# Kernel optimization log

Measured on AMD Instinct MI355X. Metric: run time of the kernel, lower is better.

Reference implementation:

```python
import jax, jax.numpy as jnp
import numpy as np

H = 2048
Q_RANK = 256
SCALE = float(np.sqrt(Q_RANK))


def setup_inputs() -> dict:
    key = jax.random.key(0)
    k_x, k_s, k_a, k_o, k_b = jax.random.split(key, 5)
    B, L = 4, 4096
    x = jax.random.normal(k_x, (B, L, H), dtype=jnp.float32)
    # nn.Linear(H, q_rank, bias=False): weight [q_rank, H]; y = x @ W.T -> store transposed [H, q_rank]
    Ws = jax.random.normal(k_s, (H, Q_RANK), dtype=jnp.float32) / np.sqrt(H)
    Wa = jax.random.normal(k_a, (H, Q_RANK), dtype=jnp.float32) / np.sqrt(H)
    Wo = jax.random.normal(k_o, (H, H), dtype=jnp.float32) / np.sqrt(H)
    bo = jax.random.normal(k_b, (H,), dtype=jnp.float32) * 0.01
    return {"x": x, "Ws": Ws, "Wa": Wa, "Wo": Wo, "bo": bo}


def reference(x, Ws, Wa, Wo, bo):
    # x: [B, L, H]
    B, L, _ = x.shape
    state = jnp.einsum('blh,hr->blr', x, Ws)   # [B, L, r]
    action = jnp.einsum('blh,hr->blr', x, Wa)  # [B, L, r]
    q_values = jnp.einsum('bir,bjr->bij', state, action) / SCALE  # [B, L, L]
    # causal mask: position i attends to j <= i
    causal = jnp.tril(jnp.ones((L, L), dtype=bool))
    q_values = jnp.where(causal, q_values, -jnp.inf)
    weights = jax.nn.softmax(q_values, axis=-1)  # [B, L, L]
    out = jnp.einsum('bij,bjh->bih', weights, x)  # weights @ x (x acts as V)
    return jnp.einsum('bih,ho->bio', out, Wo.T) + bo  # out_proj: y = out @ Wo_lin.T; Wo stored as [H,H] input-major
```

## Files before the change

### kernel.cpp

```cpp
#include <hip/hip_runtime.h>
#include <hip/hip_bf16.h>
#include <cstdint>
#include <cstddef>

typedef __bf16 bf16_t;
typedef __bf16 bf16x8 __attribute__((ext_vector_type(8)));
typedef __bf16 bf16x4v __attribute__((ext_vector_type(4)));
typedef float f32x4 __attribute__((ext_vector_type(4)));

#define B_SZ 4
#define L_SZ 4096
#define H_SZ 2048
#define R_SZ 256
#define EXP_SC 0.090168440f
#define E2_ELEMS 8912896L
#define E2_BYTES 17825792L

#define GLDS16(gaddr, laddr)                                                    \
  __builtin_amdgcn_global_load_lds(                                             \
      (const __attribute__((address_space(1))) void*)(gaddr),                   \
      (__attribute__((address_space(3))) void*)(laddr), 16, 0, 0)

__device__ __forceinline__ f32x4 mfma16(bf16x8 a, bf16x8 b, f32x4 c) {
  return __builtin_amdgcn_mfma_f32_16x16x32_bf16(a, b, c, 0, 0, 0);
}

__device__ __forceinline__ float rsum16(float v) {
  v += __shfl_xor(v, 1, 16);
  v += __shfl_xor(v, 2, 16);
  v += __shfl_xor(v, 4, 16);
  v += __shfl_xor(v, 8, 16);
  return v;
}

__global__ void cvt_x_kernel(const float* __restrict__ x, bf16_t* __restrict__ xb, int n4) {
  int i = blockIdx.x * blockDim.x + threadIdx.x;
  const int stride = gridDim.x * blockDim.x;
  for (; i < n4; i += stride) {
    float4 v = reinterpret_cast<const float4*>(x)[i];
    bf16x4v o;
    o[0] = (bf16_t)v.x; o[1] = (bf16_t)v.y; o[2] = (bf16_t)v.z; o[3] = (bf16_t)v.w;
    reinterpret_cast<bf16x4v*>(xb)[i] = o;
  }
}

__global__ void cvt_w_kernel(const float* __restrict__ Ws, const float* __restrict__ Wa,
                             const float* __restrict__ Wo,
                             bf16_t* __restrict__ Wst, bf16_t* __restrict__ Wat,
                             bf16_t* __restrict__ Wob, float* __restrict__ lsum) {
  const int tid = blockIdx.x * blockDim.x + threadIdx.x;
  const int stride = gridDim.x * blockDim.x;
  for (int idx = tid; idx < R_SZ * H_SZ; idx += stride) {
    const int rr = idx >> 11;
    const int h  = idx & (H_SZ - 1);
    Wst[idx] = (bf16_t)Ws[h * R_SZ + rr];
    Wat[idx] = (bf16_t)Wa[h * R_SZ + rr];
  }
  for (int idx = tid; idx < H_SZ * H_SZ; idx += stride) {
    Wob[idx] = (bf16_t)Wo[idx];
  }
  for (int idx = tid; idx < B_SZ * L_SZ; idx += stride) lsum[idx] = 0.0f;
}


#define G8_STG(P, REGION, BUFOFF, HALF)                                        \
  GLDS16((P)[0], lds + (REGION) + (BUFOFF) + (HALF)*16384 + ldst0);            \
  GLDS16((P)[1], lds + (REGION) + (BUFOFF) + (HALF)*16384 + ldst1);            \
  (P)[0] += 128; (P)[1] += 128;

#define G8_LDA(MH, BO) {                                                       \
  const char* ap_ = lds + (BO) + (MH)*16384;                                   \
  fa[0][0] = *(const bf16x8*)(ap_ + aOff0);                                    \
  fa[0][1] = *(const bf16x8*)(ap_ + aOff1);                                    \
  fa[1][0] = *(const bf16x8*)(ap_ + 4096 + aOff0);                             \
  fa[1][1] = *(const bf16x8*)(ap_ + 4096 + aOff1);                             \
  fa[2][0] = *(const bf16x8*)(ap_ + 8192 + aOff0);                             \
  fa[2][1] = *(const bf16x8*)(ap_ + 8192 + aOff1);                             \
  fa[3][0] = *(const bf16x8*)(ap_ + 12288 + aOff0);                            \
  fa[3][1] = *(const bf16x8*)(ap_ + 12288 + aOff1); }

#define G8_LDB(NH, BO) {                                                       \
  const char* bp_ = lds + 65536 + (BO) + (NH)*16384;                           \
  fb[NH][0][0] = *(const bf16x8*)(bp_ + bOff0);                                \
  fb[NH][0][1] = *(const bf16x8*)(bp_ + bOff1);                                \
  fb[NH][1][0] = *(const bf16x8*)(bp_ + 8192 + bOff0);                         \
  fb[NH][1][1] = *(const bf16x8*)(bp_ + 8192 + bOff1); }

#define G8_MM1(AM, AN, MF, NH, J)                                              \
  acc[AM][AN] = mfma16(fa[MF][1], fb[NH][J][1],                                \
                 mfma16(fa[MF][0], fb[NH][J][0], acc[AM][AN]))

#define G8_MM(MH, NH)                                                          \
  G8_MM1((MH)*4+0, (NH)*2+0, 0, NH, 0); G8_MM1((MH)*4+0, (NH)*2+1, 0, NH, 1); \
  G8_MM1((MH)*4+1, (NH)*2+0, 1, NH, 0); G8_MM1((MH)*4+1, (NH)*2+1, 1, NH, 1); \
  G8_MM1((MH)*4+2, (NH)*2+0, 2, NH, 0); G8_MM1((MH)*4+2, (NH)*2+1, 2, NH, 1); \
  G8_MM1((MH)*4+3, (NH)*2+0, 3, NH, 0); G8_MM1((MH)*4+3, (NH)*2+1, 3, NH, 1)

#define G8_PHASE(LOADS, STAGES, WAITS, MH, NH)                                 \
  LOADS;                                                                       \
  STAGES;                                                                      \
  __builtin_amdgcn_sched_barrier(0);                                           \
  __builtin_amdgcn_s_barrier();                                                \
  asm volatile("s_waitcnt lgkmcnt(0)" ::: "memory");                           \
  __builtin_amdgcn_sched_barrier(0);                                           \
  __builtin_amdgcn_s_setprio(1);                                               \
  G8_MM(MH, NH);                                                               \
  __builtin_amdgcn_s_setprio(0);                                               \
  WAITS;                                                                       \
  __builtin_amdgcn_sched_barrier(0);                                           \
  __builtin_amdgcn_s_barrier();

__device__ __forceinline__ void gemm8_core(
    const char* Ag, const char* Bg, long aRowB, long bRowB, int NT,
    char* lds, f32x4 (&acc)[8][4])
{
  const int t = threadIdx.x;
  const int l = t & 63;
  const int wid = t >> 6;
  const int wr = wid >> 2;
  const int wc = wid & 3;
  const int l15 = l & 15;
  const int l4 = l >> 4;
  const int swzm = (l15 & 7) << 4;
  const int aOff0 = (wr * 16 + l15) * 128 + ((l4 * 16) ^ swzm);
  const int aOff1 = (wr * 16 + l15) * 128 + ((64 + l4 * 16) ^ swzm);
  const int bOff0 = (wc * 16 + l15) * 128 + ((l4 * 16) ^ swzm);
  const int bOff1 = (wc * 16 + l15) * 128 + ((64 + l4 * 16) ^ swzm);
  const int d0 = t * 16, d1 = t * 16 + 8192;
  const int r0 = d0 >> 7, r1 = d1 >> 7;
  const int s0 = (d0 & 127) ^ ((r0 & 7) << 4);
  const int s1 = (d1 & 127) ^ ((r1 & 7) << 4);
  const char* pA0[2] = { Ag + (long)r0 * aRowB + s0, Ag + (long)r1 * aRowB + s1 };
  const char* pA1[2] = { Ag + (long)(128 + r0) * aRowB + s0, Ag + (long)(128 + r1) * aRowB + s1 };
  const char* pB0[2] = { Bg + (long)r0 * bRowB + s0, Bg + (long)r1 * bRowB + s1 };
  const char* pB1[2] = { Bg + (long)(128 + r0) * bRowB + s0, Bg + (long)(128 + r1) * bRowB + s1 };
  const int ldst0 = wid * 1024, ldst1 = wid * 1024 + 8192;
  bf16x8 fa[4][2], fb[2][2][2];

  G8_STG(pA0, 0, 0, 0);
  G8_STG(pB0, 65536, 0, 0);
  G8_STG(pA1, 0, 0, 1);
  G8_STG(pB1, 65536, 0, 1);
  G8_STG(pA0, 0, 32768, 0);
  G8_STG(pB0, 65536, 32768, 0);
  asm volatile("s_waitcnt vmcnt(4)" ::: "memory");
  __builtin_amdgcn_sched_barrier(0);
  __builtin_amdgcn_s_barrier();

  int bufOff = 0;
  for (int T = 0; T < NT - 2; ++T) {
    const int ob = bufOff ^ 32768;
    G8_PHASE(G8_LDA(0, bufOff) G8_LDB(0, bufOff), G8_STG(pA1, 0, ob, 1), , 0, 0);
    G8_PHASE(G8_LDB(1, bufOff), G8_STG(pB1, 65536, ob, 1), , 0, 1);
    G8_PHASE(G8_LDA(1, bufOff), G8_STG(pA0, 0, bufOff, 0), , 1, 0);
    G8_PHASE(, G8_STG(pB0, 65536, bufOff, 0),
             asm volatile("s_waitcnt vmcnt(4)" ::: "memory"), 1, 1);
    bufOff ^= 32768;
  }
  {
    const int ob = bufOff ^ 32768;
    G8_PHASE(G8_LDA(0, bufOff) G8_LDB(0, bufOff), G8_STG(pA1, 0, ob, 1), , 0, 0);
    G8_PHASE(G8_LDB(1, bufOff), G8_STG(pB1, 65536, ob, 1), , 0, 1);
    G8_PHASE(G8_LDA(1, bufOff), , , 1, 0);
    G8_PHASE(, , asm volatile("s_waitcnt vmcnt(0)" ::: "memory"), 1, 1);
    bufOff ^= 32768;
  }
  {
    G8_PHASE(G8_LDA(0, bufOff) G8_LDB(0, bufOff), , , 0, 0);
    G8_PHASE(G8_LDB(1, bufOff), , , 0, 1);
    G8_PHASE(G8_LDA(1, bufOff), , , 1, 0);
    G8_PHASE(, , , 1, 1);
  }
}

__global__ __launch_bounds__(512) void qk8_kernel(
    const bf16_t* __restrict__ xb, const bf16_t* __restrict__ Wst,
    const bf16_t* __restrict__ Wat, bf16_t* __restrict__ Qb, bf16_t* __restrict__ Kb)
{
  extern __shared__ char lds[];
  const long mBase = (long)blockIdx.x * 256;
  const bf16_t* W = blockIdx.z ? Wat : Wst;
  bf16_t* Cp = blockIdx.z ? Kb : Qb;
  f32x4 acc[8][4] = {};
  gemm8_core((const char*)xb + mBase * (H_SZ * 2), (const char*)W,
             H_SZ * 2, H_SZ * 2, H_SZ / 64, lds, acc);
  const int t = threadIdx.x, l = t & 63, wid = t >> 6;
  const int wr = wid >> 2, wc = wid & 3, l15 = l & 15, l4 = l >> 4;
#pragma unroll
  for (int am = 0; am < 8; ++am) {
#pragma unroll
    for (int an = 0; an < 4; ++an) {
      const long row = mBase + wr * 16 + am * 32 + l4 * 4;
      const int col = wc * 16 + an * 64 + l15;
#pragma unroll
      for (int r = 0; r < 4; ++r)
        Cp[(row + r) * R_SZ + col] = (bf16_t)acc[am][an][r];
    }
  }
}

__global__ __launch_bounds__(512) void vp8_kernel(
    const bf16_t* __restrict__ Wob, const bf16_t* __restrict__ xb, bf16_t* __restrict__ VT)
{
  extern __shared__ char lds[];
  const long mBase = (long)blockIdx.x * 256;
  const long nBase = (long)blockIdx.y * 256;
  const int b = blockIdx.z;
  f32x4 acc[8][4] = {};
  gemm8_core((const char*)Wob + mBase * (H_SZ * 2),
             (const char*)xb + ((long)b * L_SZ + nBase) * (H_SZ * 2),
             H_SZ * 2, H_SZ * 2, H_SZ / 64, lds, acc);
  bf16_t* Cp = VT + (long)b * H_SZ * L_SZ;
  const int t = threadIdx.x, l = t & 63, wid = t >> 6;
  const int wr = wid >> 2, wc = wid & 3, l15 = l & 15, l4 = l >> 4;
#pragma unroll
  for (int am = 0; am < 8; ++am) {
#pragma unroll
    for (int an = 0; an < 4; ++an) {
      const long row = mBase + wr * 16 + am * 32 + l4 * 4;
      const long col = nBase + wc * 16 + an * 64 + l15;
#pragma unroll
      for (int r = 0; r < 4; ++r)
        Cp[(row + r) * L_SZ + col] = (bf16_t)acc[am][an][r];
    }
  }
}

__global__ __launch_bounds__(256) void epass_kernel(
    const bf16_t* __restrict__ Qb, const bf16_t* __restrict__ Kb,
    bf16_t* __restrict__ E, float* __restrict__ lsum)
{
  const int mi = blockIdx.x;
  const int ji = blockIdx.y;
  if (ji > (mi | 1)) return;
  const int b = blockIdx.z;

  __shared__ __attribute__((aligned(16))) bf16_t lA[128 * 64];
  __shared__ __attribute__((aligned(16))) bf16_t lB[128 * 64];
  const int t = threadIdx.x;
  const int l = t & 63;
  const int wv = t >> 6, wr = wv >> 1, wc = wv & 1;
  const char* Ab = (const char*)(Qb + (long)b * L_SZ * R_SZ);
  const char* Bb = (const char*)(Kb + (long)b * L_SZ * R_SZ);
  const int mBase = mi * 128;
  const int nBase = ji * 128;
  const long rowBytes = R_SZ * 2;
  char* lAb = (char*)lA;
  char* lBb = (char*)lB;
  f32x4 acc[4][4] = {};

  for (int ks = 0; ks < 4; ++ks) {
    const int kbyte = ks * 128;
#pragma unroll
    for (int i = 0; i < 4; ++i) {
      const int d = t * 16 + i * 4096;
      const int row = d >> 7;
      const int src = (d & 127) ^ ((row & 7) << 4);
      const int ldst = wv * 1024 + i * 4096;
      GLDS16(Ab + (long)(mBase + row) * rowBytes + kbyte + src, lAb + ldst);
      GLDS16(Bb + (long)(nBase + row) * rowBytes + kbyte + src, lBb + ldst);
    }
    __syncthreads();
#pragma unroll
    for (int kk = 0; kk < 2; ++kk) {
      bf16x8 af[4], bfv[4];
#pragma unroll
      for (int mt = 0; mt < 4; ++mt) {
        const int row = wr * 64 + mt * 16 + (l & 15);
        const int inr = (kk * 64 + ((l >> 4) * 16)) ^ ((row & 7) << 4);
        af[mt] = *(const bf16x8*)(lAb + row * 128 + inr);
      }
#pragma unroll
      for (int nt = 0; nt < 4; ++nt) {
        const int row = wc * 64 + nt * 16 + (l & 15);
        const int inr = (kk * 64 + ((l >> 4) * 16)) ^ ((row & 7) << 4);
        bfv[nt] = *(const bf16x8*)(lBb + row * 128 + inr);
      }
#pragma unroll
      for (int mt = 0; mt < 4; ++mt)
#pragma unroll
        for (int nt = 0; nt < 4; ++nt)
          acc[mt][nt] = mfma16(af[mt], bfv[nt], acc[mt][nt]);
    }
    __syncthreads();
  }

  const int P = mi >> 1;
  bf16_t* Ep = E + (long)b * E2_ELEMS + 32768L * P * (P + 1);
  const long ldaE = (P + 1) * 256;
  const int rbase = (mi & 1) * 128;
  const int l15 = l & 15;
  const int lrow = (l >> 4) * 4;
#pragma unroll
  for (int mt = 0; mt < 4; ++mt) {
#pragma unroll
    for (int r = 0; r < 4; ++r) {
      const int row_in = wr * 64 + mt * 16 + lrow + r;
      const int ii = mBase + row_in;
      float s = 0.0f;
#pragma unroll
      for (int nt = 0; nt < 4; ++nt) {
        const int col_in = wc * 64 + nt * 16 + l15;
        const int jj = nBase + col_in;
        float p = exp2f(acc[mt][nt][r] * EXP_SC);
        if (jj > ii) p = 0.0f;
        Ep[(long)(rbase + row_in) * ldaE + ji * 128 + col_in] = (bf16_t)p;
        s += p;
      }
      s = rsum16(s);
      if (l15 == 0) atomicAdd(lsum + (long)b * L_SZ + ii, s);
    }
  }
}

__global__ __launch_bounds__(512) void pv8_kernel(
    const bf16_t* __restrict__ E, const bf16_t* __restrict__ VT,
    const float* __restrict__ lsum, const float* __restrict__ bo,
    float* __restrict__ out)
{
  extern __shared__ char lds[];
  const int pr = blockIdx.x;
  const int nBase = blockIdx.y * 256;
  const int b = blockIdx.z;
  const int t = threadIdx.x, l = t & 63, wid = t >> 6;
  const int wr = wid >> 2, wc = wid & 3, l15 = l & 15, l4 = l >> 4;

#pragma unroll
  for (int s = 0; s < 2; ++s) {
    const int mt = s ? pr : (15 - pr);
    f32x4 acc[8][4] = {};
    const char* Ag = (const char*)E + (long)b * E2_BYTES + 65536L * mt * (mt + 1);
    const char* Bg = (const char*)VT + ((long)b * H_SZ + nBase) * (L_SZ * 2);
    gemm8_core(Ag, Bg, (long)(mt + 1) * 512, L_SZ * 2, (mt + 1) * 4, lds, acc);
#pragma unroll
    for (int am = 0; am < 8; ++am) {
      const long rowG = (long)b * L_SZ + mt * 256 + wr * 16 + am * 32 + l4 * 4;
      float linv[4];
#pragma unroll
      for (int r = 0; r < 4; ++r) linv[r] = 1.0f / lsum[rowG + r];
#pragma unroll
      for (int an = 0; an < 4; ++an) {
        const int col = nBase + wc * 16 + an * 64 + l15;
        const float bias = bo[col];
#pragma unroll
        for (int r = 0; r < 4; ++r)
          out[(rowG + r) * H_SZ + col] = acc[am][an][r] * linv[r] + bias;
      }
    }
  }
}

extern "C" void kernel_launch(void* const* d_in, const int* in_sizes, int n_in,
                              void* d_out, int out_size, void* d_ws, size_t ws_size,
                              hipStream_t stream) {
  const float* x  = (const float*)d_in[0];
  const float* Ws = (const float*)d_in[1];
  const float* Wa = (const float*)d_in[2];
  const float* Wo = (const float*)d_in[3];
  const float* bo = (const float*)d_in[4];
  float* out = (float*)d_out;

  char* ws = (char*)d_ws;
  bf16_t* xb  = (bf16_t*)(ws + 0);
  bf16_t* Wst = (bf16_t*)(ws + 67108864);
  bf16_t* Wat = (bf16_t*)(ws + 68157440);
  bf16_t* Wob = (bf16_t*)(ws + 69206016);
  bf16_t* Qb  = (bf16_t*)(ws + 77594624);
  bf16_t* Kb  = (bf16_t*)(ws + 85983232);
  bf16_t* VT  = (bf16_t*)(ws + 94371840);
  float*  lsum = (float*)(ws + 161480704);
  bf16_t* E   = (bf16_t*)(ws + 0);

  hipFuncSetAttribute((const void*)qk8_kernel, hipFuncAttributeMaxDynamicSharedMemorySize, 131072);
  hipFuncSetAttribute((const void*)vp8_kernel, hipFuncAttributeMaxDynamicSharedMemorySize, 131072);
  hipFuncSetAttribute((const void*)pv8_kernel, hipFuncAttributeMaxDynamicSharedMemorySize, 131072);

  cvt_x_kernel<<<dim3(2048), dim3(256), 0, stream>>>(x, xb, B_SZ * L_SZ * H_SZ / 4);
  cvt_w_kernel<<<dim3(1024), dim3(256), 0, stream>>>(Ws, Wa, Wo, Wst, Wat, Wob, lsum);
  qk8_kernel<<<dim3(64, 1, 2), dim3(512), 131072, stream>>>(xb, Wst, Wat, Qb, Kb);
  vp8_kernel<<<dim3(8, 16, 4), dim3(512), 131072, stream>>>(Wob, xb, VT);
  epass_kernel<<<dim3(32, 32, 4), dim3(256), 0, stream>>>(Qb, Kb, E, lsum);
  pv8_kernel<<<dim3(8, 8, 4), dim3(512), 131072, stream>>>(E, VT, lsum, bo, out);
}
```

Baseline: 416.2 us.

## Retile score pass onto shared 256x256 GEMM core and remap block order for XCDs

The score/exp kernel now runs on the same 512-thread 256x256 gemm8_core used by the other GEMMs, replacing the 128x128 tile kernel. Causal masking is applied only on diagonal tiles, and blocks above the diagonal no longer do the partial-tile work they did under the old mi|1 rule. The vp8 and pv8 launches are flattened to 1D grids with a permuted block index, so consecutive blocks dispatched round-robin across XCDs share operands in L2. The larger tiles cut launch count and reload traffic but leave fewer active blocks and use 128 KB of LDS each.

```diff
diff --git a/kernel.cpp b/kernel.cpp
--- a/kernel.cpp
+++ b/kernel.cpp
@@ -203,9 +203,13 @@
     const bf16_t* __restrict__ Wob, const bf16_t* __restrict__ xb, bf16_t* __restrict__ VT)
 {
   extern __shared__ char lds[];
-  const long mBase = (long)blockIdx.x * 256;
-  const long nBase = (long)blockIdx.y * 256;
-  const int b = blockIdx.z;
+  const int f = blockIdx.x;
+  const int lg = (f & 7) * 64 + (f >> 3);
+  const int xo = lg & 7;
+  const int yj = (lg >> 3) & 15;
+  const int b  = lg >> 7;
+  const long mBase = (long)xo * 256;
+  const long nBase = (long)yj * 256;
   f32x4 acc[8][4] = {};
   gemm8_core((const char*)Wob + mBase * (H_SZ * 2),
              (const char*)xb + ((long)b * L_SZ + nBase) * (H_SZ * 2),
@@ -226,89 +230,41 @@
   }
 }
 
-__global__ __launch_bounds__(256) void epass_kernel(
+__global__ __launch_bounds__(512) void ep8_kernel(
     const bf16_t* __restrict__ Qb, const bf16_t* __restrict__ Kb,
     bf16_t* __restrict__ E, float* __restrict__ lsum)
 {
-  const int mi = blockIdx.x;
-  const int ji = blockIdx.y;
-  if (ji > (mi | 1)) return;
+  extern __shared__ char lds[];
+  const int P = blockIdx.x;
+  const int Jp = blockIdx.y;
+  if (Jp > P) return;
   const int b = blockIdx.z;
-
-  __shared__ __attribute__((aligned(16))) bf16_t lA[128 * 64];
-  __shared__ __attribute__((aligned(16))) bf16_t lB[128 * 64];
-  const int t = threadIdx.x;
-  const int l = t & 63;
-  const int wv = t >> 6, wr = wv >> 1, wc = wv & 1;
-  const char* Ab = (const char*)(Qb + (long)b * L_SZ * R_SZ);
-  const char* Bb = (const char*)(Kb + (long)b * L_SZ * R_SZ);
-  const int mBase = mi * 128;
-  const int nBase = ji * 128;
-  const long rowBytes = R_SZ * 2;
-  char* lAb = (char*)lA;
-  char* lBb = (char*)lB;
-  f32x4 acc[4][4] = {};
-
-  for (int ks = 0; ks < 4; ++ks) {
-    const int kbyte = ks * 128;
-#pragma unroll
-    for (int i = 0; i < 4; ++i) {
-      const int d = t * 16 + i * 4096;
-      const int row = d >> 7;
-      const int src = (d & 127) ^ ((row & 7) << 4);
-      const int ldst = wv * 1024 + i * 4096;
-      GLDS16(Ab + (long)(mBase + row) * rowBytes + kbyte + src, lAb + ldst);
-      GLDS16(Bb + (long)(nBase + row) * rowBytes + kbyte + src, lBb + ldst);
-    }
-    __syncthreads();
-#pragma unroll
-    for (int kk = 0; kk < 2; ++kk) {
-      bf16x8 af[4], bfv[4];
-#pragma unroll
-      for (int mt = 0; mt < 4; ++mt) {
-        const int row = wr * 64 + mt * 16 + (l & 15);
-        const int inr = (kk * 64 + ((l >> 4) * 16)) ^ ((row & 7) << 4);
-        af[mt] = *(const bf16x8*)(lAb + row * 128 + inr);
-      }
-#pragma unroll
-      for (int nt = 0; nt < 4; ++nt) {
-        const int row = wc * 64 + nt * 16 + (l & 15);
-        const int inr = (kk * 64 + ((l >> 4) * 16)) ^ ((row & 7) << 4);
-        bfv[nt] = *(const bf16x8*)(lBb + row * 128 + inr);
-      }
-#pragma unroll
-      for (int mt = 0; mt < 4; ++mt)
-#pragma unroll
-        for (int nt = 0; nt < 4; ++nt)
-          acc[mt][nt] = mfma16(af[mt], bfv[nt], acc[mt][nt]);
-    }
-    __syncthreads();
-  }
-
-  const int P = mi >> 1;
+  f32x4 acc[8][4] = {};
+  gemm8_core((const char*)Qb + ((long)b * L_SZ + P * 256) * (R_SZ * 2),
+             (const char*)Kb + ((long)b * L_SZ + Jp * 256) * (R_SZ * 2),
+             R_SZ * 2, R_SZ * 2, R_SZ / 64, lds, acc);
+  const int t = threadIdx.x, l = t & 63, wid = t >> 6;
+  const int wr = wid >> 2, wc = wid & 3, l15 = l & 15, l4 = l >> 4;
   bf16_t* Ep = E + (long)b * E2_ELEMS + 32768L * P * (P + 1);
-  const long ldaE = (P + 1) * 256;
-  const int rbase = (mi & 1) * 128;
-  const int l15 = l & 15;
-  const int lrow = (l >> 4) * 4;
-#pragma unroll
-  for (int mt = 0; mt < 4; ++mt) {
+  const long ldaE = (long)(P + 1) * 256;
+  float* lp = lsum + (long)b * L_SZ + P * 256;
+  const bool diag = (Jp == P);
+#pragma unroll
+  for (int am = 0; am < 8; ++am) {
+    const int rowi = wr * 16 + am * 32 + l4 * 4;
 #pragma unroll
     for (int r = 0; r < 4; ++r) {
-      const int row_in = wr * 64 + mt * 16 + lrow + r;
-      const int ii = mBase + row_in;
       float s = 0.0f;
 #pragma unroll
-      for (int nt = 0; nt < 4; ++nt) {
-        const int col_in = wc * 64 + nt * 16 + l15;
-        const int jj = nBase + col_in;
-        float p = exp2f(acc[mt][nt][r] * EXP_SC);
-        if (jj > ii) p = 0.0f;
-        Ep[(long)(rbase + row_in) * ldaE + ji * 128 + col_in] = (bf16_t)p;
+      for (int an = 0; an < 4; ++an) {
+        const int coli = wc * 16 + an * 64 + l15;
+        float p = exp2f(acc[am][an][r] * EXP_SC);
+        if (diag && coli > rowi + r) p = 0.0f;
+        Ep[(long)(rowi + r) * ldaE + Jp * 256 + coli] = (bf16_t)p;
         s += p;
       }
       s = rsum16(s);
-      if (l15 == 0) atomicAdd(lsum + (long)b * L_SZ + ii, s);
+      if (l15 == 0) atomicAdd(lp + rowi + r, s);
     }
   }
 }
@@ -319,9 +275,12 @@
     float* __restrict__ out)
 {
   extern __shared__ char lds[];
-  const int pr = blockIdx.x;
-  const int nBase = blockIdx.y * 256;
-  const int b = blockIdx.z;
+  const int f = blockIdx.x;
+  const int lg = (f & 7) * 32 + (f >> 3);
+  const int yj = lg & 7;
+  const int pr = (lg >> 3) & 7;
+  const int b  = lg >> 6;
+  const int nBase = yj * 256;
   const int t = threadIdx.x, l = t & 63, wid = t >> 6;
   const int wr = wid >> 2, wc = wid & 3, l15 = l & 15, l4 = l >> 4;
 
@@ -373,12 +332,13 @@
 
   hipFuncSetAttribute((const void*)qk8_kernel, hipFuncAttributeMaxDynamicSharedMemorySize, 131072);
   hipFuncSetAttribute((const void*)vp8_kernel, hipFuncAttributeMaxDynamicSharedMemorySize, 131072);
+  hipFuncSetAttribute((const void*)ep8_kernel, hipFuncAttributeMaxDynamicSharedMemorySize, 131072);
   hipFuncSetAttribute((const void*)pv8_kernel, hipFuncAttributeMaxDynamicSharedMemorySize, 131072);
 
   cvt_x_kernel<<<dim3(2048), dim3(256), 0, stream>>>(x, xb, B_SZ * L_SZ * H_SZ / 4);
   cvt_w_kernel<<<dim3(1024), dim3(256), 0, stream>>>(Ws, Wa, Wo, Wst, Wat, Wob, lsum);
   qk8_kernel<<<dim3(64, 1, 2), dim3(512), 131072, stream>>>(xb, Wst, Wat, Qb, Kb);
-  vp8_kernel<<<dim3(8, 16, 4), dim3(512), 131072, stream>>>(Wob, xb, VT);
-  epass_kernel<<<dim3(32, 32, 4), dim3(256), 0, stream>>>(Qb, Kb, E, lsum);
-  pv8_kernel<<<dim3(8, 8, 4), dim3(512), 131072, stream>>>(E, VT, lsum, bo, out);
-}
+  vp8_kernel<<<dim3(512, 1, 1), dim3(512), 131072, stream>>>(Wob, xb, VT);
+  ep8_kernel<<<dim3(16, 16, 4), dim3(512), 131072, stream>>>(Qb, Kb, E, lsum);
+  pv8_kernel<<<dim3(256, 1, 1), dim3(512), 131072, stream>>>(E, VT, lsum, bo, out);
+}
```

New measurement: 410.3 us. Within noise of the previous version (-1.4%).
